# Optimization experiments

Measured on AMD Instinct MI355X. Metric: run time of the kernel, lower is better.

## Reference

```python
import jax, jax.numpy as jnp
import numpy as np
import math

B, S, D = 4, 2048, 1024
H, KV = 16, 4
HD = D // H
GROUPS = H // KV

def _alibi_slopes(n):
    # n assumed power of 2 here (n=16)
    start = 2.0 ** (-2.0 ** (-(math.log2(n) - 3)))
    return np.array([start * start ** i for i in range(n)], dtype=np.float32)

def setup_inputs() -> dict:
    key = jax.random.key(0)
    ks = jax.random.split(key, 5)
    sc = 0.02
    return {
        "x": jax.random.normal(ks[0], (B, S, D), jnp.float32),
        "Wq": jax.random.normal(ks[1], (D, H * HD), jnp.float32) * sc,
        "Wk": jax.random.normal(ks[2], (D, KV * HD), jnp.float32) * sc,
        "Wv": jax.random.normal(ks[3], (D, KV * HD), jnp.float32) * sc,
        "Wo": jax.random.normal(ks[4], (H * HD, D), jnp.float32) * sc,
    }

def reference(x, Wq, Wk, Wv, Wo):
    b, s, _ = x.shape
    scale = HD ** -0.5
    q = (x @ Wq).reshape(b, s, H, HD).transpose(0, 2, 1, 3)   # [b,H,s,hd]
    k = (x @ Wk).reshape(b, s, KV, HD).transpose(0, 2, 1, 3)  # [b,KV,s,hd]
    v = (x @ Wv).reshape(b, s, KV, HD).transpose(0, 2, 1, 3)
    k = jnp.repeat(k, GROUPS, axis=1)  # [b,H,s,hd]
    v = jnp.repeat(v, GROUPS, axis=1)
    attn = jnp.einsum('bhqd,bhkd->bhqk', q, k) * scale
    # ALiBi bias: slope_h * (j - i)
    slopes = jnp.asarray(_alibi_slopes(H))
    pos = jnp.arange(s, dtype=jnp.float32)
    rel = pos[None, :] - pos[:, None]                     # [s,s]
    attn = attn + slopes[None, :, None, None] * rel[None, None, :, :]
    attn = jax.nn.softmax(attn, axis=-1)
    out = jnp.einsum('bhqk,bhkd->bhqd', attn, v)
    out = out.transpose(0, 2, 1, 3).reshape(b, s, H * HD)
    return out @ Wo
```

## Files before the change

kernel.cpp:

```cpp
#include <hip/hip_runtime.h>

typedef unsigned short u16;
typedef unsigned int u32;
typedef unsigned char u8;
typedef _Float16 f16;
typedef __attribute__((ext_vector_type(8))) f16 f16x8;
typedef __attribute__((ext_vector_type(4))) float f32x4;

#define S_LEN 2048
#define DM 1024
#define QKVW 1536
#define KVSTRIDE (S_LEN * 64)

__device__ __forceinline__ u16 f2h(float x) {
    f16 h = (f16)x;
    return __builtin_bit_cast(u16, h);
}

__device__ __forceinline__ void g2l16(const void* g, void* l) {
    __builtin_amdgcn_global_load_lds((const __attribute__((address_space(1))) u32*)g,
                                     (__attribute__((address_space(3))) u32*)l, 16, 0, 0);
}

__global__ __launch_bounds__(256)
void prep(const float* __restrict__ x, u16* __restrict__ xh,
          const float* __restrict__ Wq, const float* __restrict__ Wk,
          const float* __restrict__ Wv, const float* __restrict__ Wo,
          u16* __restrict__ Wtq, u16* __restrict__ Wto) {
    __shared__ float tbuf[32][33];
    const int tid = threadIdx.x;
    const int blk = blockIdx.x;
    if (blk < 8192) {
        int i = blk * 256 + tid;
        float4 v = ((const float4*)x)[i];
        ((ushort4*)xh)[i] = make_ushort4(f2h(v.x), f2h(v.y), f2h(v.z), f2h(v.w));
        return;
    }
    int t = blk - 8192;
    const float* src;
    u16* dst;
    int C, cx, ry;
    if (t < 1024)      { src = Wq; dst = Wtq;               C = 1024; cx = t & 31; ry = t >> 5; }
    else if (t < 1280) { t -= 1024; src = Wk; dst = Wtq + 1024 * 1024; C = 256; cx = t & 7; ry = t >> 3; }
    else if (t < 1536) { t -= 1280; src = Wv; dst = Wtq + 1280 * 1024; C = 256; cx = t & 7; ry = t >> 3; }
    else               { t -= 1536; src = Wo; dst = Wto;    C = 1024; cx = t & 31; ry = t >> 5; }
    const int c0 = cx * 32, r0 = ry * 32;
    const int tx = tid & 31, ty = tid >> 5;
#pragma unroll
    for (int i = 0; i < 4; ++i)
        tbuf[ty + 8 * i][tx] = src[(long)(r0 + ty + 8 * i) * C + c0 + tx];
    __syncthreads();
#pragma unroll
    for (int i = 0; i < 4; ++i)
        dst[(long)(c0 + ty + 8 * i) * 1024 + r0 + tx] = f2h(tbuf[tx][ty + 8 * i]);
}

template <bool FUSED>
__global__ __launch_bounds__(256, 3)
void gemm_bt(const u16* __restrict__ A, const u16* __restrict__ Bt,
             float* __restrict__ Cf, u16* __restrict__ Qp,
             u16* __restrict__ Kp, u16* __restrict__ Vp, int N, int K) {
    __shared__ __attribute__((aligned(16))) u16 sA[128 * 32];
    __shared__ __attribute__((aligned(16))) u16 sB[128 * 32];
    const int tid = threadIdx.x, w = tid >> 6, lane = tid & 63;
    const int quad = lane >> 4, l15 = lane & 15;
    const int wm = w & 1, wn = w >> 1;
    const long row0 = (long)blockIdx.x * 128, col0 = (long)blockIdx.y * 128;

    f32x4 acc[4][4];
#pragma unroll
    for (int mb = 0; mb < 4; ++mb)
#pragma unroll
        for (int nb = 0; nb < 4; ++nb) acc[mb][nb] = (f32x4){0.f, 0.f, 0.f, 0.f};

    const int r = lane >> 2;
    const int cch = (lane & 3) ^ (r & 3);

    for (int kt = 0; kt < K; kt += 32) {
        __syncthreads();
#pragma unroll
        for (int i = 0; i < 4; ++i) {
            int gid = w + 4 * i;
            int buf = gid >> 3, seg = gid & 7;
            const u16* src = buf ? Bt : A;
            long base0 = buf ? col0 : row0;
            const u16* g = src + (base0 + seg * 16 + r) * (long)K + kt + cch * 8;
            u16* dst = (buf ? sB : sA) + seg * 512;
            g2l16(g, dst);
        }
        __syncthreads();

        f16x8 bfr[4];
#pragma unroll
        for (int nb = 0; nb < 4; ++nb) {
            int rr = wn * 64 + nb * 16 + l15;
            bfr[nb] = *(const f16x8*)(sB + rr * 32 + ((quad ^ (l15 & 3)) * 8));
        }
#pragma unroll
        for (int mb = 0; mb < 4; ++mb) {
            int rr = wm * 64 + mb * 16 + l15;
            f16x8 af = *(const f16x8*)(sA + rr * 32 + ((quad ^ (l15 & 3)) * 8));
#pragma unroll
            for (int nb = 0; nb < 4; ++nb)
                acc[mb][nb] = __builtin_amdgcn_mfma_f32_16x16x32_f16(af, bfr[nb], acc[mb][nb], 0, 0, 0);
        }
    }

    if constexpr (FUSED) {
        const int bq = (int)(row0 >> 11);
        u16* kpbat = Kp + (long)bq * 4 * KVSTRIDE;
        u16* vpbat = Vp + (long)bq * 4 * KVSTRIDE;
#pragma unroll
        for (int mb = 0; mb < 4; ++mb) {
            const int key0 = ((int)(row0 & 2047)) + wm * 64 + mb * 16 + quad * 4;
#pragma unroll
            for (int nb = 0; nb < 4; ++nb) {
                const int colbase = (int)col0 + wn * 64 + nb * 16;
                if (colbase < 1024) {
#pragma unroll
                    for (int rr = 0; rr < 4; ++rr) {
                        long row = row0 + wm * 64 + mb * 16 + quad * 4 + rr;
                        Qp[row * 1024 + colbase + l15] = f2h(acc[mb][nb][rr]);
                    }
                } else if (colbase < 1280) {
                    const int cc = colbase - 1024;
                    const int d = (cc & 63) + l15;
                    u16* kp = kpbat + (long)(cc >> 6) * KVSTRIDE;
                    const int dpart = (d >> 5) * 512 + ((d >> 3) & 3) * 128 + (d & 7);
#pragma unroll
                    for (int rr = 0; rr < 4; ++rr) {
                        int key = key0 + rr;
                        kp[(key >> 4) * 1024 + (key & 15) * 8 + dpart] = f2h(acc[mb][nb][rr]);
                    }
                } else {
                    const int cc = colbase - 1280;
                    const int d = (cc & 63) + l15;
                    u16* vp = vpbat + (long)(cc >> 6) * KVSTRIDE;
                    const long idx = (long)((key0 >> 5) * 4 + (d >> 4)) * 512 +
                                     ((key0 >> 3) & 3) * 128 + (d & 15) * 8 + (key0 & 7);
                    ushort4 pk = make_ushort4(f2h(acc[mb][nb][0]), f2h(acc[mb][nb][1]),
                                              f2h(acc[mb][nb][2]), f2h(acc[mb][nb][3]));
                    *(ushort4*)(vp + idx) = pk;
                }
            }
        }
    } else {
#pragma unroll
        for (int mb = 0; mb < 4; ++mb)
#pragma unroll
            for (int nb = 0; nb < 4; ++nb)
#pragma unroll
                for (int rr = 0; rr < 4; ++rr) {
                    long row = row0 + wm * 64 + mb * 16 + quad * 4 + rr;
                    long col = col0 + wn * 64 + nb * 16 + l15;
                    Cf[row * N + col] = acc[mb][nb][rr];
                }
    }
}

__device__ const u8 UH[21]  = {15,15,14,14,13,13,12,10,12,11,11, 9, 8, 7, 6, 5, 4, 3, 2, 1, 0};
__device__ const u8 UK0[21] = { 0,16, 0,16, 0,16, 1,16,17,10,21,21,24,26,28,29,30,30,31,31,31};
__device__ const u8 UK1[21] = {16,32,16,32,16,32,17,32,32,21,32,32,32,32,32,32,32,32,32,32,32};
__device__ const u8 UC[21]  = { 0, 1, 0, 1, 0, 1, 0, 0, 1, 0, 1, 0, 0, 0, 0, 0, 0, 0, 0, 0, 0};

__global__ __launch_bounds__(256, 4)
void attn(const u16* __restrict__ Qp, const u16* __restrict__ Kp,
          const u16* __restrict__ Vp, u16* __restrict__ Oh,
          float* __restrict__ Of, float* __restrict__ Ls) {
    __shared__ __attribute__((aligned(16))) u16 sP[2][4][16][72];
    const int tid = threadIdx.x, w = tid >> 6, lane = tid & 63;
    const int quad = lane >> 4, l15 = lane & 15;

    const int id = blockIdx.x;
    const int u = id >> 6, s = id & 63;
    const int b = s >> 4, qt = s & 15;
    const int h = UH[u];
    const int kt0 = UK0[u], kt1 = UK1[u];
    const int chunk = UC[u];
    const bool split = (u <= 10) && (u != 7);
    const int kvh = h >> 2;

    const float c1 = 0.125f * 1.44269504f;
    const float c2 = __builtin_amdgcn_exp2f(-0.5f * (float)(h + 1)) * 1.44269504f;
    const float d0 = -8.0f - c2 * 2047.0f;

    const long qrow0 = (long)b * S_LEN + qt * 128 + w * 32;

    f16x8 qf[2][2];
#pragma unroll
    for (int rg = 0; rg < 2; ++rg)
#pragma unroll
        for (int ch = 0; ch < 2; ++ch)
            qf[rg][ch] = *(const f16x8*)(Qp + (qrow0 + rg * 16 + l15) * 1024 +
                                         h * 64 + ch * 32 + quad * 8);

    f32x4 oacc[2][4];
    float lsum[2][4];
#pragma unroll
    for (int rg = 0; rg < 2; ++rg) {
#pragma unroll
        for (int nb = 0; nb < 4; ++nb) oacc[rg][nb] = (f32x4){0.f, 0.f, 0.f, 0.f};
#pragma unroll
        for (int rr = 0; rr < 4; ++rr) lsum[rg][rr] = 0.f;
    }

    const u16* kpb = Kp + (long)(b * 4 + kvh) * KVSTRIDE + lane * 8;
    const u16* vpb = Vp + (long)(b * 4 + kvh) * KVSTRIDE + lane * 8;

    for (int kt = kt0; kt < kt1; ++kt) {
        __builtin_amdgcn_s_barrier();
        f16x8 kf[8];
#pragma unroll
        for (int j = 0; j < 8; ++j)
            kf[j] = *(const f16x8*)(kpb + (long)(kt * 8 + j) * 512);
        const float kcb = fmaf(c2, (float)(kt * 64 + l15), d0);
#pragma unroll
        for (int rg = 0; rg < 2; ++rg) {
#pragma unroll
            for (int kb = 0; kb < 4; ++kb) {
                f32x4 z = (f32x4){0.f, 0.f, 0.f, 0.f};
                z = __builtin_amdgcn_mfma_f32_16x16x32_f16(qf[rg][0], kf[2 * kb], z, 0, 0, 0);
                z = __builtin_amdgcn_mfma_f32_16x16x32_f16(qf[rg][1], kf[2 * kb + 1], z, 0, 0, 0);
                float kc = fmaf(c2, (float)(16 * kb), kcb);
#pragma unroll
                for (int rr = 0; rr < 4; ++rr) {
                    float p = __builtin_amdgcn_exp2f(fmaf(z[rr], c1, kc));
                    lsum[rg][rr] += p;
                    sP[rg][w][quad * 4 + rr][kb * 16 + l15] = f2h(p);
                }
            }
        }
        f16x8 vf[8];
#pragma unroll
        for (int j = 0; j < 8; ++j)
            vf[j] = *(const f16x8*)(vpb + (long)(kt * 8 + j) * 512);
#pragma unroll
        for (int rg = 0; rg < 2; ++rg)
#pragma unroll
            for (int ch = 0; ch < 2; ++ch) {
                f16x8 pf = *(const f16x8*)(&sP[rg][w][l15][ch * 32 + quad * 8]);
#pragma unroll
                for (int nb = 0; nb < 4; ++nb)
                    oacc[rg][nb] = __builtin_amdgcn_mfma_f32_16x16x32_f16(pf, vf[ch * 4 + nb],
                                                                          oacc[rg][nb], 0, 0, 0);
            }
    }

#pragma unroll
    for (int rg = 0; rg < 2; ++rg) {
        float red[4];
#pragma unroll
        for (int rr = 0; rr < 4; ++rr) {
            float v = lsum[rg][rr];
#pragma unroll
            for (int off = 1; off < 16; off <<= 1) v += __shfl_xor(v, off, 64);
            red[rr] = v;
        }
        if (split) {
            const int hs = h - 11;
#pragma unroll
            for (int rr = 0; rr < 4; ++rr) {
                long rowg = qrow0 + rg * 16 + quad * 4 + rr;
                if (l15 == 0)
                    Ls[(long)(chunk * 8192) * 5 + rowg * 5 + hs] = red[rr];
#pragma unroll
                for (int nb = 0; nb < 4; ++nb)
                    Of[((long)(chunk * 8192) + rowg) * 320 + hs * 64 + nb * 16 + l15] =
                        oacc[rg][nb][rr];
            }
        } else {
#pragma unroll
            for (int nb = 0; nb < 4; ++nb)
#pragma unroll
                for (int rr = 0; rr < 4; ++rr) {
                    long row = qrow0 + rg * 16 + quad * 4 + rr;
                    long col = h * 64 + nb * 16 + l15;
                    Oh[row * DM + col] = f2h(oacc[rg][nb][rr] / red[rr]);
                }
        }
    }
}

__global__ __launch_bounds__(256)
void norm_split(const float* __restrict__ Of, const float* __restrict__ Ls,
                u16* __restrict__ Oh) {
    const int gid = blockIdx.x * 256 + threadIdx.x;
    const int d4 = gid & 15;
    const int rh = gid >> 4;
    const int hs = rh % 5;
    const int row = rh / 5;
    const float l = Ls[rh] + Ls[rh + 40960];
    const float4 a = ((const float4*)Of)[rh * 16 + d4];
    const float4 bq = ((const float4*)Of)[(rh + 40960) * 16 + d4];
    const float inv = 1.0f / l;
    const int col = (hs + 11) * 64 + d4 * 4;
    ((ushort4*)(Oh + (long)row * DM + col))[0] =
        make_ushort4(f2h((a.x + bq.x) * inv), f2h((a.y + bq.y) * inv),
                     f2h((a.z + bq.z) * inv), f2h((a.w + bq.w) * inv));
}

extern "C" void kernel_launch(void* const* d_in, const int* in_sizes, int n_in,
                              void* d_out, int out_size, void* d_ws, size_t ws_size,
                              hipStream_t stream) {
    const float* x = (const float*)d_in[0];
    const float* Wq = (const float*)d_in[1];
    const float* Wk = (const float*)d_in[2];
    const float* Wv = (const float*)d_in[3];
    const float* Wo = (const float*)d_in[4];
    char* ws = (char*)d_ws;
    const size_t MB = 1 << 20;

    u16* xh = (u16*)ws;
    u16* Wtq = (u16*)(ws + 16 * MB);
    u16* Wto = (u16*)(ws + 19 * MB);
    u16* Qp = (u16*)(ws + 21 * MB);
    u16* Kp = (u16*)(ws + 37 * MB);
    u16* Vp = (u16*)(ws + 41 * MB);
    u16* Oh = xh;

    float* Of = (float*)d_out;
    float* Ls = Of + 2 * 8192 * 5 * 64;

    prep<<<10752, 256, 0, stream>>>(x, xh, Wq, Wk, Wv, Wo, Wtq, Wto);
    gemm_bt<true><<<dim3(64, 12), 256, 0, stream>>>(xh, Wtq, nullptr, Qp, Kp, Vp, QKVW, 1024);
    attn<<<1344, 256, 0, stream>>>(Qp, Kp, Vp, Oh, Of, Ls);
    norm_split<<<2560, 256, 0, stream>>>(Of, Ls, Oh);
    gemm_bt<false><<<dim3(64, 8), 256, 0, stream>>>(Oh, Wto, (float*)d_out, nullptr, nullptr, nullptr, 1024, 1024);
}
```

Baseline: 199.6 us.

## Double-buffer V tiles in LDS and prefetch next K tile into registers

The attention loop now stages V tiles into a double-buffered shared-memory array with async global-to-LDS loads issued one iteration ahead. K fragments for the next tile are loaded into registers right after the QK MFMAs, so their latency overlaps with the exp/softmax work. The idea is to hide global-load latency that was previously exposed at each iteration. In exchange it adds 16KB of LDS per block, a full __syncthreads per iteration, and redundant last-iteration loads, which may reduce occupancy at the 4-blocks-per-CU launch bound.

```diff
diff --git a/kernel.cpp b/kernel.cpp
--- a/kernel.cpp
+++ b/kernel.cpp
@@ -168,6 +168,7 @@
           const u16* __restrict__ Vp, u16* __restrict__ Oh,
           float* __restrict__ Of, float* __restrict__ Ls) {
     __shared__ __attribute__((aligned(16))) u16 sP[2][4][16][72];
+    __shared__ __attribute__((aligned(16))) u16 sV[2][4096];
     const int tid = threadIdx.x, w = tid >> 6, lane = tid & 63;
     const int quad = lane >> 4, l15 = lane & 15;
 
@@ -205,45 +206,77 @@
     }
 
     const u16* kpb = Kp + (long)(b * 4 + kvh) * KVSTRIDE + lane * 8;
-    const u16* vpb = Vp + (long)(b * 4 + kvh) * KVSTRIDE + lane * 8;
+    const u16* vtb = Vp + (long)(b * 4 + kvh) * KVSTRIDE;
+
+    f16x8 kf[8];
+#pragma unroll
+    for (int j = 0; j < 8; ++j)
+        kf[j] = *(const f16x8*)(kpb + (long)(kt0 * 8 + j) * 512);
+    {
+        const u16* src = vtb + (long)kt0 * 4096;
+        u16* dst = &sV[kt0 & 1][0];
+        g2l16(src + w * 512 + lane * 8, dst + w * 512);
+        g2l16(src + (4 + w) * 512 + lane * 8, dst + (4 + w) * 512);
+    }
 
     for (int kt = kt0; kt < kt1; ++kt) {
-        __builtin_amdgcn_s_barrier();
-        f16x8 kf[8];
+        const int ktv = (kt + 1 < kt1) ? kt + 1 : kt;
+        {
+            const u16* src = vtb + (long)ktv * 4096;
+            u16* dst = &sV[(kt + 1) & 1][0];
+            g2l16(src + w * 512 + lane * 8, dst + w * 512);
+            g2l16(src + (4 + w) * 512 + lane * 8, dst + (4 + w) * 512);
+        }
+
+        f32x4 z[2][4];
+#pragma unroll
+        for (int rg = 0; rg < 2; ++rg)
+#pragma unroll
+            for (int kb = 0; kb < 4; ++kb) {
+                f32x4 zz = (f32x4){0.f, 0.f, 0.f, 0.f};
+                zz = __builtin_amdgcn_mfma_f32_16x16x32_f16(qf[rg][0], kf[2 * kb], zz, 0, 0, 0);
+                zz = __builtin_amdgcn_mfma_f32_16x16x32_f16(qf[rg][1], kf[2 * kb + 1], zz, 0, 0, 0);
+                z[rg][kb] = zz;
+            }
+        const int ktn = (kt + 1 < kt1) ? kt + 1 : kt;
 #pragma unroll
         for (int j = 0; j < 8; ++j)
-            kf[j] = *(const f16x8*)(kpb + (long)(kt * 8 + j) * 512);
+            kf[j] = *(const f16x8*)(kpb + (long)(ktn * 8 + j) * 512);
+
         const float kcb = fmaf(c2, (float)(kt * 64 + l15), d0);
 #pragma unroll
-        for (int rg = 0; rg < 2; ++rg) {
+        for (int rg = 0; rg < 2; ++rg)
 #pragma unroll
             for (int kb = 0; kb < 4; ++kb) {
-                f32x4 z = (f32x4){0.f, 0.f, 0.f, 0.f};
-                z = __builtin_amdgcn_mfma_f32_16x16x32_f16(qf[rg][0], kf[2 * kb], z, 0, 0, 0);
-                z = __builtin_amdgcn_mfma_f32_16x16x32_f16(qf[rg][1], kf[2 * kb + 1], z, 0, 0, 0);
                 float kc = fmaf(c2, (float)(16 * kb), kcb);
 #pragma unroll
                 for (int rr = 0; rr < 4; ++rr) {
-                    float p = __builtin_amdgcn_exp2f(fmaf(z[rr], c1, kc));
+                    float p = __builtin_amdgcn_exp2f(fmaf(z[rg][kb][rr], c1, kc));
                     lsum[rg][rr] += p;
                     sP[rg][w][quad * 4 + rr][kb * 16 + l15] = f2h(p);
                 }
             }
-        }
-        f16x8 vf[8];
-#pragma unroll
-        for (int j = 0; j < 8; ++j)
-            vf[j] = *(const f16x8*)(vpb + (long)(kt * 8 + j) * 512);
-#pragma unroll
-        for (int rg = 0; rg < 2; ++rg)
-#pragma unroll
-            for (int ch = 0; ch < 2; ++ch) {
+
+        __syncthreads();
+
+        const u16* sVq = &sV[kt & 1][0];
+#pragma unroll
+        for (int ch = 0; ch < 2; ++ch) {
+            f16x8 vv[4];
+#pragma unroll
+            for (int nb = 0; nb < 4; ++nb)
+                vv[nb] = *(const f16x8*)(sVq + (ch * 4 + nb) * 512 + lane * 8);
+#pragma unroll
+            for (int rg = 0; rg < 2; ++rg) {
                 f16x8 pf = *(const f16x8*)(&sP[rg][w][l15][ch * 32 + quad * 8]);
 #pragma unroll
                 for (int nb = 0; nb < 4; ++nb)
-                    oacc[rg][nb] = __builtin_amdgcn_mfma_f32_16x16x32_f16(pf, vf[ch * 4 + nb],
+                    oacc[rg][nb] = __builtin_amdgcn_mfma_f32_16x16x32_f16(pf, vv[nb],
                                                                           oacc[rg][nb], 0, 0, 0);
             }
+        }
+
+        __builtin_amdgcn_s_barrier();
     }
 
 #pragma unroll
```

Result: slower. 226.4 us (+13.5%).

## Double-buffer K/V tiles in LDS via async global_load_lds prefetch

Applied to the files above, without the earlier changes.

Before, each wave read the K and V tiles straight from global memory into registers, so all four waves issued duplicate loads. Now the block cooperatively stages each 64-key K/V tile into double-buffered LDS with global_load_lds, prefetching the next tile while computing the current one. Waves then read the tile from LDS. MFMA sections are wrapped in s_setprio to favour matrix issue. This adds LDS footprint (32KB more), lowers the occupancy hint from 4 to 3 blocks per CU, and replaces the loop-top barrier with a full __syncthreads at the end of each iteration.

```diff
diff --git a/kernel.cpp b/kernel.cpp
--- a/kernel.cpp
+++ b/kernel.cpp
@@ -163,11 +163,13 @@
 __device__ const u8 UK1[21] = {16,32,16,32,16,32,17,32,32,21,32,32,32,32,32,32,32,32,32,32,32};
 __device__ const u8 UC[21]  = { 0, 1, 0, 1, 0, 1, 0, 0, 1, 0, 1, 0, 0, 0, 0, 0, 0, 0, 0, 0, 0};
 
-__global__ __launch_bounds__(256, 4)
+__global__ __launch_bounds__(256, 3)
 void attn(const u16* __restrict__ Qp, const u16* __restrict__ Kp,
           const u16* __restrict__ Vp, u16* __restrict__ Oh,
           float* __restrict__ Of, float* __restrict__ Ls) {
     __shared__ __attribute__((aligned(16))) u16 sP[2][4][16][72];
+    __shared__ __attribute__((aligned(16))) u16 sK[2][4096];
+    __shared__ __attribute__((aligned(16))) u16 sV[2][4096];
     const int tid = threadIdx.x, w = tid >> 6, lane = tid & 63;
     const int quad = lane >> 4, l15 = lane & 15;
 
@@ -204,23 +206,47 @@
         for (int rr = 0; rr < 4; ++rr) lsum[rg][rr] = 0.f;
     }
 
-    const u16* kpb = Kp + (long)(b * 4 + kvh) * KVSTRIDE + lane * 8;
-    const u16* vpb = Vp + (long)(b * 4 + kvh) * KVSTRIDE + lane * 8;
-
+    const u16* ktb = Kp + (long)(b * 4 + kvh) * KVSTRIDE;
+    const u16* vtb = Vp + (long)(b * 4 + kvh) * KVSTRIDE;
+
+    {
+        const u16* ksrc = ktb + (long)kt0 * 4096;
+        const u16* vsrc = vtb + (long)kt0 * 4096;
+        g2l16(ksrc + w * 512 + lane * 8,       &sK[0][w * 512]);
+        g2l16(ksrc + (4 + w) * 512 + lane * 8, &sK[0][(4 + w) * 512]);
+        g2l16(vsrc + w * 512 + lane * 8,       &sV[0][w * 512]);
+        g2l16(vsrc + (4 + w) * 512 + lane * 8, &sV[0][(4 + w) * 512]);
+    }
+    __syncthreads();
+
+    int cur = 0;
     for (int kt = kt0; kt < kt1; ++kt) {
-        __builtin_amdgcn_s_barrier();
+        if (kt + 1 < kt1) {
+            const int nxt = cur ^ 1;
+            const u16* ksrc = ktb + (long)(kt + 1) * 4096;
+            const u16* vsrc = vtb + (long)(kt + 1) * 4096;
+            g2l16(ksrc + w * 512 + lane * 8,       &sK[nxt][w * 512]);
+            g2l16(ksrc + (4 + w) * 512 + lane * 8, &sK[nxt][(4 + w) * 512]);
+            g2l16(vsrc + w * 512 + lane * 8,       &sV[nxt][w * 512]);
+            g2l16(vsrc + (4 + w) * 512 + lane * 8, &sV[nxt][(4 + w) * 512]);
+        }
+
+        const u16* sKc = &sK[cur][0];
         f16x8 kf[8];
 #pragma unroll
         for (int j = 0; j < 8; ++j)
-            kf[j] = *(const f16x8*)(kpb + (long)(kt * 8 + j) * 512);
+            kf[j] = *(const f16x8*)(sKc + j * 512 + lane * 8);
+
         const float kcb = fmaf(c2, (float)(kt * 64 + l15), d0);
 #pragma unroll
         for (int rg = 0; rg < 2; ++rg) {
 #pragma unroll
             for (int kb = 0; kb < 4; ++kb) {
                 f32x4 z = (f32x4){0.f, 0.f, 0.f, 0.f};
+                __builtin_amdgcn_s_setprio(1);
                 z = __builtin_amdgcn_mfma_f32_16x16x32_f16(qf[rg][0], kf[2 * kb], z, 0, 0, 0);
                 z = __builtin_amdgcn_mfma_f32_16x16x32_f16(qf[rg][1], kf[2 * kb + 1], z, 0, 0, 0);
+                __builtin_amdgcn_s_setprio(0);
                 float kc = fmaf(c2, (float)(16 * kb), kcb);
 #pragma unroll
                 for (int rr = 0; rr < 4; ++rr) {
@@ -230,20 +256,27 @@
                 }
             }
         }
+
+        const u16* sVc = &sV[cur][0];
         f16x8 vf[8];
 #pragma unroll
         for (int j = 0; j < 8; ++j)
-            vf[j] = *(const f16x8*)(vpb + (long)(kt * 8 + j) * 512);
+            vf[j] = *(const f16x8*)(sVc + j * 512 + lane * 8);
 #pragma unroll
         for (int rg = 0; rg < 2; ++rg)
 #pragma unroll
             for (int ch = 0; ch < 2; ++ch) {
                 f16x8 pf = *(const f16x8*)(&sP[rg][w][l15][ch * 32 + quad * 8]);
+                __builtin_amdgcn_s_setprio(1);
 #pragma unroll
                 for (int nb = 0; nb < 4; ++nb)
                     oacc[rg][nb] = __builtin_amdgcn_mfma_f32_16x16x32_f16(pf, vf[ch * 4 + nb],
                                                                           oacc[rg][nb], 0, 0, 0);
+                __builtin_amdgcn_s_setprio(0);
             }
+
+        __syncthreads();
+        cur ^= 1;
     }
 
 #pragma unroll
```

Result: no change. 203.2 us (+1.8%).
